# Optimization experiments

Measured on AMD Instinct MI355X. Metric: run time of the kernel, lower is better.

Reference implementation:

```python
import jax, jax.numpy as jnp
import numpy as np

N = 50000
E = 800000
IN_CH = 128
OUT_CH = 32
HEADS = 2
NEG_SLOPE = 0.2


def setup_inputs() -> dict:
    key = jax.random.key(0)
    k_x, k_ei, k_w, k_as, k_ad, k_b = jax.random.split(key, 6)
    x = jax.random.normal(k_x, (N, IN_CH), dtype=jnp.float32)
    edge_index = jax.random.randint(k_ei, (2, E), 0, N, dtype=jnp.int64)
    # Glorot-style init scale for linear weight and attention vectors
    w_scale = 1.0 / np.sqrt(IN_CH)
    W = jax.random.normal(k_w, (IN_CH, HEADS * OUT_CH), dtype=jnp.float32) * w_scale
    a_scale = 1.0 / np.sqrt(OUT_CH)
    a_src = jax.random.normal(k_as, (HEADS, OUT_CH), dtype=jnp.float32) * a_scale
    a_dst = jax.random.normal(k_ad, (HEADS, OUT_CH), dtype=jnp.float32) * a_scale
    bias = jnp.zeros((HEADS * OUT_CH,), dtype=jnp.float32)
    return {"x": x, "edge_index": edge_index, "W": W, "a_src": a_src,
            "a_dst": a_dst, "bias": bias}


def reference(x, edge_index, W, a_src, a_dst, bias):
    n = x.shape[0]
    # add self-loops (add_self_loops=True); static shape E+N
    loops = jnp.tile(jnp.arange(n, dtype=edge_index.dtype), (2, 1))
    ei = jnp.concatenate([edge_index, loops], axis=1)
    src, dst = ei[0], ei[1]

    # linear projection -> per-head features [N, H, C]
    h = (x @ W).reshape(n, HEADS, OUT_CH)

    # per-node attention logits [N, H]
    alpha_s = jnp.sum(h * a_src[None], axis=-1)
    alpha_d = jnp.sum(h * a_dst[None], axis=-1)

    # per-edge score, LeakyReLU, segment softmax over edges grouped by dst
    e = jax.nn.leaky_relu(alpha_s[src] + alpha_d[dst], NEG_SLOPE)  # [E', H]
    e_max = jax.ops.segment_max(e, dst, num_segments=n)           # [N, H]
    e_exp = jnp.exp(e - e_max[dst])
    denom = jax.ops.segment_sum(e_exp, dst, num_segments=n)       # [N, H]
    alpha = e_exp / (denom[dst] + 1e-16)                          # [E', H]

    # scatter-add weighted messages [N, H, C]
    out = jax.ops.segment_sum(alpha[:, :, None] * h[src], dst, num_segments=n)
    # concat heads + bias (concat=True)
    return out.reshape(n, HEADS * OUT_CH) + bias
```

## Files before the change

kernel.cpp:

```cpp
#include <hip/hip_runtime.h>
#include <hip/hip_bf16.h>
#include <hip/hip_fp16.h>
#include <math.h>

#define IN_CH   128
#define OUT_CH  32
#define HEADS   2
#define HC      (HEADS * OUT_CH)
#define NEG_SLOPE 0.2f

#define NODE_TILE 64
#define X_STRIDE  132

#define BIN_CAP 64

__global__ __launch_bounds__(256) void gemm_hist_kernel(
    const float* __restrict__ x, const float* __restrict__ W,
    const float* __restrict__ a_src, const float* __restrict__ a_dst,
    __half* __restrict__ h, float* __restrict__ alpha_s, float* __restrict__ alpha_d,
    const int* __restrict__ dst, int* __restrict__ deg, int* __restrict__ rank,
    int n_nodes, int n_edges, int n_total, int gemm_blocks)
{
    const int tid = threadIdx.x;

    if (blockIdx.x >= gemm_blocks) {
        int e = (blockIdx.x - gemm_blocks) * blockDim.x + tid;
        if (e < n_total) {
            int d = (e < n_edges) ? dst[e] : (e - n_edges);
            rank[e] = atomicAdd(&deg[d], 1);
        }
        return;
    }

    __shared__ float Ws[IN_CH * HC];
    __shared__ float Xs[NODE_TILE * X_STRIDE];

    const int node0 = blockIdx.x * NODE_TILE;

    const float4* W4 = (const float4*)W;
    float4* Ws4 = (float4*)Ws;
    #pragma unroll
    for (int i = 0; i < 8; ++i) Ws4[tid + i * 256] = W4[tid + i * 256];

    const float4* X4 = (const float4*)x;
    #pragma unroll
    for (int i = 0; i < 8; ++i) {
        int idx = tid + i * 256;
        int r = idx >> 5, c4 = idx & 31;
        int node = node0 + r;
        float4 v = make_float4(0.f, 0.f, 0.f, 0.f);
        if (node < n_nodes) v = X4[(size_t)node * (IN_CH / 4) + c4];
        *(float4*)&Xs[r * X_STRIDE + c4 * 4] = v;
    }
    __syncthreads();

    const int n    = tid >> 3;
    const int g    = tid & 7;
    const int col0 = g * 8;
    const int head = col0 >> 5;
    const int c0   = col0 & 31;

    float accA[8] = {0,0,0,0,0,0,0,0};
    float accB[8] = {0,0,0,0,0,0,0,0};
    const float* xa = &Xs[n * X_STRIDE];
    const float* xb = &Xs[(n + 32) * X_STRIDE];
    #pragma unroll 8
    for (int k = 0; k < IN_CH; ++k) {
        float va = xa[k], vb = xb[k];
        const float4 w0 = *(const float4*)&Ws[k * HC + col0];
        const float4 w1 = *(const float4*)&Ws[k * HC + col0 + 4];
        accA[0] += va * w0.x; accA[1] += va * w0.y;
        accA[2] += va * w0.z; accA[3] += va * w0.w;
        accA[4] += va * w1.x; accA[5] += va * w1.y;
        accA[6] += va * w1.z; accA[7] += va * w1.w;
        accB[0] += vb * w0.x; accB[1] += vb * w0.y;
        accB[2] += vb * w0.z; accB[3] += vb * w0.w;
        accB[4] += vb * w1.x; accB[5] += vb * w1.y;
        accB[6] += vb * w1.z; accB[7] += vb * w1.w;
    }

    float asr[8], adr[8];
    #pragma unroll
    for (int j = 0; j < 8; ++j) {
        asr[j] = a_src[head * OUT_CH + c0 + j];
        adr[j] = a_dst[head * OUT_CH + c0 + j];
    }

    #pragma unroll
    for (int half = 0; half < 2; ++half) {
        const float* acc = half ? accB : accA;
        const int node = node0 + n + half * 32;
        if (node < n_nodes) {
            unsigned u[8];
            #pragma unroll
            for (int j = 0; j < 8; ++j) u[j] = __half_as_ushort(__float2half_rn(acc[j]));
            int4 v = make_int4((int)(u[0] | (u[1] << 16)), (int)(u[2] | (u[3] << 16)),
                               (int)(u[4] | (u[5] << 16)), (int)(u[6] | (u[7] << 16)));
            *(int4*)&h[(size_t)node * HC + col0] = v;
        }
        float ps = 0.f, pd = 0.f;
        #pragma unroll
        for (int j = 0; j < 8; ++j) { ps += acc[j] * asr[j]; pd += acc[j] * adr[j]; }
        ps += __shfl_xor(ps, 1); ps += __shfl_xor(ps, 2);
        pd += __shfl_xor(pd, 1); pd += __shfl_xor(pd, 2);
        if ((g & 3) == 0 && node < n_nodes) {
            alpha_s[node * HEADS + head] = ps;
            alpha_d[node * HEADS + head] = pd;
        }
    }
}

__global__ void fill_kernel(const int* __restrict__ src, const int* __restrict__ dst,
                            const int* __restrict__ rank,
                            const float* __restrict__ alpha_s, const float* __restrict__ alpha_d,
                            int2* __restrict__ bins, int n_edges, int n_total)
{
    int e = blockIdx.x * blockDim.x + threadIdx.x;
    if (e >= n_total) return;
    int s, d;
    if (e < n_edges) { s = src[e]; d = dst[e]; }
    else             { s = d = e - n_edges; }
    float2 as = ((const float2*)alpha_s)[s];
    float2 ad = ((const float2*)alpha_d)[d];
    int rk = rank[e];
    float v0 = as.x + ad.x;
    float v1 = as.y + ad.y;
    v0 = (v0 > 0.f) ? v0 : NEG_SLOPE * v0;
    v1 = (v1 > 0.f) ? v1 : NEG_SLOPE * v1;
    unsigned u0 = __half_as_ushort(__float2half_rn(__expf(v0)));
    unsigned u1 = __half_as_ushort(__float2half_rn(__expf(v1)));
    if (rk < BIN_CAP) {
        int2 rec;
        rec.x = s;
        rec.y = (int)((u1 << 16) | u0);
        bins[(size_t)d * BIN_CAP + rk] = rec;
    }
}

__device__ __forceinline__ float unpack_p(int py, int head) {
    unsigned u = (unsigned)py;
    unsigned short us = (unsigned short)(head ? (u >> 16) : (u & 0xffffu));
    return __half2float(__ushort_as_half(us));
}

__global__ __launch_bounds__(256) void node_gather_kernel(
    const int2* __restrict__ bins, const int* __restrict__ deg,
    const __half* __restrict__ h, const float* __restrict__ bias,
    float* __restrict__ out, int n_nodes)
{
    int node = blockIdx.x * (blockDim.x >> 6) + (threadIdx.x >> 6);
    if (node >= n_nodes) return;
    const int lane = threadIdx.x & 63;
    const int head = lane >> 5;
    int cnt = deg[node];
    if (cnt > BIN_CAP) cnt = BIN_CAP;
    const int2* ep = bins + (size_t)node * BIN_CAP;

    int rx = 0, ry = 0;
    if (lane < cnt) { int2 r = ep[lane]; rx = r.x; ry = r.y; }

    float acc = 0.f, lsum = 0.f;
    for (int i = 0; i < cnt; i += 8) {
        #pragma unroll
        for (int j = 0; j < 8; ++j) {
            int idx = i + j;
            int sj = __shfl(rx, idx);
            int yj = __shfl(ry, idx);
            float pj = (idx < cnt) ? unpack_p(yj, head) : 0.f;
            float hj = __half2float(h[(size_t)sj * HC + lane]);
            acc += pj * hj;
            lsum += pj;
        }
    }
    out[(size_t)node * HC + lane] = acc / (lsum + 1e-16f) + bias[lane];
}

extern "C" void kernel_launch(void* const* d_in, const int* in_sizes, int n_in,
                              void* d_out, int out_size, void* d_ws, size_t ws_size,
                              hipStream_t stream)
{
    const float* x      = (const float*)d_in[0];
    const int*   ei     = (const int*)d_in[1];
    const float* W      = (const float*)d_in[2];
    const float* a_src  = (const float*)d_in[3];
    const float* a_dst  = (const float*)d_in[4];
    const float* bias   = (const float*)d_in[5];
    float* out = (float*)d_out;

    const int n_nodes = in_sizes[0] / IN_CH;
    const int n_edges = in_sizes[1] / 2;
    const int n_total = n_edges + n_nodes;

    const int* src = ei;
    const int* dst = ei + n_edges;

    __half* h      = (__half*)d_ws;
    float* alpha_s = (float*)(h + (size_t)n_nodes * HC);
    float* alpha_d = alpha_s + (size_t)n_nodes * HEADS;
    int* deg       = (int*)(alpha_d + (size_t)n_nodes * HEADS);
    int* rank      = deg + n_nodes;
    uintptr_t ep   = (uintptr_t)(rank + n_total);
    ep = (ep + 15) & ~(uintptr_t)15;
    int2* bins     = (int2*)ep;

    const int edge_blocks = (n_total + 255) / 256;
    const int gemm_blocks = (n_nodes + NODE_TILE - 1) / NODE_TILE;

    hipMemsetAsync(deg, 0, (size_t)n_nodes * sizeof(int), stream);

    gemm_hist_kernel<<<gemm_blocks + edge_blocks, 256, 0, stream>>>(
        x, W, a_src, a_dst, h, alpha_s, alpha_d,
        dst, deg, rank, n_nodes, n_edges, n_total, gemm_blocks);

    fill_kernel<<<edge_blocks, 256, 0, stream>>>(
        src, dst, rank, alpha_s, alpha_d, bins, n_edges, n_total);

    int ng_blocks = (n_nodes + 3) / 4;
    node_gather_kernel<<<ng_blocks, 256, 0, stream>>>(
        bins, deg, h, bias, out, n_nodes);
}
```

Baseline: 171.2 us.

## Use fp16 dot2 for projection GEMM with transposed W in LDS; unroll gather 16

The projection GEMM now converts x and W to fp16 in shared memory, stores W transposed with a padded stride, and accumulates with packed fp16 dot2 instructions into fp32. This halves LDS footprint and read traffic and doubles math per instruction in the GEMM part of the fused kernel. The node gather loop is unrolled to 16 edges per iteration to expose more outstanding loads. The cost is reduced input precision for the projection and slightly more wasted work for low-degree nodes.

Measured after the change: 163.9 us. 1.04x faster.

```diff
diff --git a/kernel.cpp b/kernel.cpp
--- a/kernel.cpp
+++ b/kernel.cpp
@@ -10,9 +10,20 @@
 #define NEG_SLOPE 0.2f
 
 #define NODE_TILE 64
-#define X_STRIDE  132
+#define LDS_STRIDE 136
 
 #define BIN_CAP 64
+
+typedef _Float16 h2_t __attribute__((ext_vector_type(2)));
+union V16 { int4 v; h2_t h[4]; };
+
+__device__ __forceinline__ float fdot2(h2_t a, h2_t b, float c) {
+#if __has_builtin(__builtin_amdgcn_fdot2)
+    return __builtin_amdgcn_fdot2(a, b, c, false);
+#else
+    return c + (float)a.x * (float)b.x + (float)a.y * (float)b.y;
+#endif
+}
 
 __global__ __launch_bounds__(256) void gemm_hist_kernel(
     const float* __restrict__ x, const float* __restrict__ W,
@@ -32,25 +43,34 @@
         return;
     }
 
-    __shared__ float Ws[IN_CH * HC];
-    __shared__ float Xs[NODE_TILE * X_STRIDE];
+    __shared__ _Float16 Wt[HC * LDS_STRIDE];
+    __shared__ _Float16 Xs[NODE_TILE * LDS_STRIDE];
 
     const int node0 = blockIdx.x * NODE_TILE;
 
     const float4* W4 = (const float4*)W;
-    float4* Ws4 = (float4*)Ws;
-    #pragma unroll
-    for (int i = 0; i < 8; ++i) Ws4[tid + i * 256] = W4[tid + i * 256];
+    #pragma unroll
+    for (int i = 0; i < 8; ++i) {
+        int idx4 = tid + i * 256;
+        int k  = idx4 >> 4;
+        int c4 = idx4 & 15;
+        float4 v = W4[idx4];
+        Wt[(c4 * 4 + 0) * LDS_STRIDE + k] = (_Float16)v.x;
+        Wt[(c4 * 4 + 1) * LDS_STRIDE + k] = (_Float16)v.y;
+        Wt[(c4 * 4 + 2) * LDS_STRIDE + k] = (_Float16)v.z;
+        Wt[(c4 * 4 + 3) * LDS_STRIDE + k] = (_Float16)v.w;
+    }
 
     const float4* X4 = (const float4*)x;
     #pragma unroll
     for (int i = 0; i < 8; ++i) {
-        int idx = tid + i * 256;
-        int r = idx >> 5, c4 = idx & 31;
+        int idx4 = tid + i * 256;
+        int r = idx4 >> 5, c4 = idx4 & 31;
         int node = node0 + r;
         float4 v = make_float4(0.f, 0.f, 0.f, 0.f);
         if (node < n_nodes) v = X4[(size_t)node * (IN_CH / 4) + c4];
-        *(float4*)&Xs[r * X_STRIDE + c4 * 4] = v;
+        _Float16 hv[4] = {(_Float16)v.x, (_Float16)v.y, (_Float16)v.z, (_Float16)v.w};
+        *(int2*)&Xs[r * LDS_STRIDE + c4 * 4] = *(int2*)hv;
     }
     __syncthreads();
 
@@ -62,21 +82,24 @@
 
     float accA[8] = {0,0,0,0,0,0,0,0};
     float accB[8] = {0,0,0,0,0,0,0,0};
-    const float* xa = &Xs[n * X_STRIDE];
-    const float* xb = &Xs[(n + 32) * X_STRIDE];
-    #pragma unroll 8
-    for (int k = 0; k < IN_CH; ++k) {
-        float va = xa[k], vb = xb[k];
-        const float4 w0 = *(const float4*)&Ws[k * HC + col0];
-        const float4 w1 = *(const float4*)&Ws[k * HC + col0 + 4];
-        accA[0] += va * w0.x; accA[1] += va * w0.y;
-        accA[2] += va * w0.z; accA[3] += va * w0.w;
-        accA[4] += va * w1.x; accA[5] += va * w1.y;
-        accA[6] += va * w1.z; accA[7] += va * w1.w;
-        accB[0] += vb * w0.x; accB[1] += vb * w0.y;
-        accB[2] += vb * w0.z; accB[3] += vb * w0.w;
-        accB[4] += vb * w1.x; accB[5] += vb * w1.y;
-        accB[6] += vb * w1.z; accB[7] += vb * w1.w;
+    const _Float16* xa = &Xs[n * LDS_STRIDE];
+    const _Float16* xb = &Xs[(n + 32) * LDS_STRIDE];
+
+    for (int k0 = 0; k0 < IN_CH; k0 += 8) {
+        V16 va, vb;
+        va.v = *(const int4*)&xa[k0];
+        vb.v = *(const int4*)&xb[k0];
+        #pragma unroll
+        for (int j = 0; j < 8; ++j) {
+            V16 w;
+            w.v = *(const int4*)&Wt[(col0 + j) * LDS_STRIDE + k0];
+            float a = accA[j], b = accB[j];
+            a = fdot2(w.h[0], va.h[0], a); b = fdot2(w.h[0], vb.h[0], b);
+            a = fdot2(w.h[1], va.h[1], a); b = fdot2(w.h[1], vb.h[1], b);
+            a = fdot2(w.h[2], va.h[2], a); b = fdot2(w.h[2], vb.h[2], b);
+            a = fdot2(w.h[3], va.h[3], a); b = fdot2(w.h[3], vb.h[3], b);
+            accA[j] = a; accB[j] = b;
+        }
     }
 
     float asr[8], adr[8];
@@ -160,9 +183,9 @@
     if (lane < cnt) { int2 r = ep[lane]; rx = r.x; ry = r.y; }
 
     float acc = 0.f, lsum = 0.f;
-    for (int i = 0; i < cnt; i += 8) {
+    for (int i = 0; i < cnt; i += 16) {
         #pragma unroll
-        for (int j = 0; j < 8; ++j) {
+        for (int j = 0; j < 16; ++j) {
             int idx = i + j;
             int sj = __shfl(rx, idx);
             int yj = __shfl(ry, idx);
```
